# Optimization experiments

Hardware: AMD Instinct MI355X
Metric: run time of the kernel (lower is better)

## Reference

```python
import jax, jax.numpy as jnp
import numpy as np

MARGIN = 1.0
EPS = 1e-11


def setup_inputs() -> dict:
    key = jax.random.key(0)
    k1, k2, k3 = jax.random.split(key, 3)
    B, D, C = 8192, 512, 128
    features = jax.random.normal(k1, (B, D), dtype=jnp.float32)
    labels = jax.random.randint(k2, (B,), 0, C, dtype=jnp.int64)
    neg_u = jax.random.uniform(k3, (B,), dtype=jnp.float32)
    return {"features": features, "labels": labels, "neg_u": neg_u}


def reference(features, labels, neg_u):
    n = features.shape[0]
    sq = jnp.sum(features * features, axis=1)  # [n]
    d2 = sq[:, None] + sq[None, :] - 2.0 * (features @ features.T)
    dist = jnp.sqrt(jnp.clip(d2, EPS, None))  # [n, n]

    same = labels[:, None] == labels[None, :]
    eye = jnp.eye(n, dtype=bool)
    pos_mask = same & ~eye           # valid positives per anchor
    neg_mask = ~same                 # valid negatives per anchor
    n_neg = neg_mask.sum(axis=1)     # [n]

    # deterministic "random" negative: pick the floor(u * n_neg)-th negative
    # (stable argsort puts negatives first, preserving original order)
    order = jnp.argsort(jnp.where(neg_mask, 0, 1), axis=1, stable=True)  # [n, n]
    k = jnp.floor(neg_u * n_neg.astype(neg_u.dtype)).astype(jnp.int32)
    k = jnp.clip(k, 0, jnp.maximum(n_neg - 1, 0).astype(jnp.int32))
    neg_idx = jnp.take_along_axis(order, k[:, None], axis=1)[:, 0]       # [n]
    neg_dist = dist[jnp.arange(n), neg_idx]                               # [n]

    # MarginRankingLoss(y=1): max(0, margin + pos_dist - neg_dist), per (anchor, pos) pair
    valid = pos_mask & (n_neg > 0)[:, None]
    per_pair = jnp.maximum(MARGIN + dist - neg_dist[:, None], 0.0)
    counter = valid.sum()
    total = jnp.where(valid, per_pair, 0.0).sum()
    return total / counter.astype(total.dtype)
```

## Files before the change

### kernel.cpp

```cpp
#include <hip/hip_runtime.h>
#include <hip/hip_bf16.h>
#include <cstdint>

#define NN 8192
#define DD 512
#define NC 128

typedef unsigned short u16;
typedef __attribute__((ext_vector_type(8))) short short8;
typedef __attribute__((ext_vector_type(4))) float f32x4;

#define AS1 __attribute__((address_space(1)))
#define AS3 __attribute__((address_space(3)))

__device__ __forceinline__ float bf2f(short x) {
  return __uint_as_float(((unsigned)(unsigned short)x) << 16);
}

#define FB_OFF   ((size_t)0)
#define SQ_OFF   (FB_OFF + (size_t)NN*DD*2)
#define ND_OFF   (SQ_OFF + (size_t)NN*4)
#define ACC_OFF  (ND_OFF + (size_t)NN*4)
#define CC_OFF   (ACC_OFF + 64)
#define POS_OFF  (CC_OFF + 1024)

__global__ __launch_bounds__(256) void k_pc(const float* __restrict__ F,
    const int* __restrict__ labels, u16* __restrict__ Fb,
    float* __restrict__ sq, int* __restrict__ cc, int* __restrict__ pos) {
  const int wid = threadIdx.x >> 6, lane = threadIdx.x & 63;
  if (blockIdx.x < 2048) {
    const int row = blockIdx.x * 4 + wid;
    const float* fr = F + (size_t)row * DD + lane * 8;
    float4 v0 = *(const float4*)fr;
    float4 v1 = *(const float4*)(fr + 4);
    float s = v0.x*v0.x + v0.y*v0.y + v0.z*v0.z + v0.w*v0.w
            + v1.x*v1.x + v1.y*v1.y + v1.z*v1.z + v1.w*v1.w;
    #pragma unroll
    for (int o = 32; o; o >>= 1) s += __shfl_xor(s, o);
    float t[8] = {v0.x, v0.y, v0.z, v0.w, v1.x, v1.y, v1.z, v1.w};
    unsigned p[8];
    #pragma unroll
    for (int e = 0; e < 8; ++e) {
      unsigned b = __float_as_uint(t[e]);
      b += 0x7fffu + ((b >> 16) & 1u);
      p[e] = b >> 16;
    }
    uint4 w;
    w.x = p[0] | (p[1] << 16); w.y = p[2] | (p[3] << 16);
    w.z = p[4] | (p[5] << 16); w.w = p[6] | (p[7] << 16);
    *(uint4*)(Fb + (size_t)row * DD + lane * 8) = w;
    if (lane == 0) sq[row] = s;
  } else {
    const int c = blockIdx.x - 2048;
    __shared__ int wcnt[4], woff[4];
    const int base0 = wid * 2048;
    int cw = 0;
    for (int b = 0; b < 2048; b += 64)
      cw += __popcll(__ballot(labels[base0 + b + lane] == c));
    if (lane == 0) wcnt[wid] = cw;
    __syncthreads();
    if (threadIdx.x == 0) {
      int o = 0;
      #pragma unroll
      for (int w = 0; w < 4; ++w) { woff[w] = o; o += wcnt[w]; }
      cc[c] = o;
    }
    __syncthreads();
    int off = woff[wid];
    for (int b = 0; b < 2048; b += 64) {
      const int idx = base0 + b + lane;
      const int hit = (labels[idx] == c);
      const unsigned long long m = __ballot(hit);
      if (hit) pos[c * 128 + off + __popcll(m & ((1ull << lane) - 1ull))] = idx;
      off += __popcll(m);
    }
    __syncthreads();
    const int nc = cc[c];
    for (int t = nc + threadIdx.x; t < 128; t += 256) pos[c * 128 + t] = 0;
  }
}

__global__ __launch_bounds__(256) void k_neg2(const u16* __restrict__ Fb,
    const float* __restrict__ sq, const int* __restrict__ labels,
    const float* __restrict__ negu, const int* __restrict__ cc,
    const int* __restrict__ pos, float* __restrict__ nd,
    int* __restrict__ accz) {
  if (blockIdx.x == 0 && threadIdx.x < 16) accz[threadIdx.x] = 0;
  const int wid = threadIdx.x >> 6, lane = threadIdx.x & 63;
  const int i = blockIdx.x * 4 + wid;
  const int c = labels[i];
  const int nc = cc[c];
  const int n_neg = NN - nc;
  if (n_neg <= 0) { if (lane == 0) nd[i] = __builtin_inff(); return; }
  int k = (int)floorf(negu[i] * (float)n_neg);
  k = k < 0 ? 0 : (k > n_neg - 1 ? n_neg - 1 : k);
  const int* pc = pos + c * 128;
  const int p0 = pc[lane], p1 = pc[64 + lane];
  const int t = __popcll(__ballot((lane < nc) && (p0 - lane <= k)))
              + __popcll(__ballot((64 + lane < nc) && (p1 - (64 + lane) <= k)));
  const int j = k + t;
  const short8 av = *(const short8*)(Fb + (size_t)i * DD + lane * 8);
  const short8 bv = *(const short8*)(Fb + (size_t)j * DD + lane * 8);
  float d = 0.0f;
  #pragma unroll
  for (int e = 0; e < 8; ++e) d += bf2f(av[e]) * bf2f(bv[e]);
  #pragma unroll
  for (int o = 32; o; o >>= 1) d += __shfl_xor(d, o);
  if (lane == 0) nd[i] = sqrtf(fmaxf(sq[i] + sq[j] - 2.0f * d, 1e-11f));
}

__global__ __launch_bounds__(256) void k_cls(const u16* __restrict__ Fb,
    const float* __restrict__ sq, const float* __restrict__ nd,
    const int* __restrict__ cc, const int* __restrict__ pos,
    float* __restrict__ accf, float* __restrict__ out) {
  const int c = blockIdx.x >> 1, half = blockIdx.x & 1;
  __shared__ __align__(16) u16 P[128 * 512];
  __shared__ int posc[128];
  __shared__ float red[4];
  const int tid = threadIdx.x, wid = tid >> 6, lane = tid & 63;
  const int nc = cc[c];
  if (tid < 128) posc[tid] = pos[c * 128 + tid];
  __syncthreads();
  if (nc >= 2 && half * 64 < nc) {
    const int wr = half, wc = wid;
    const int r16 = lane & 15, gg = lane >> 4;
    const char* fb = (const char*)Fb;

    #pragma unroll 8
    for (int s = 0; s < 32; ++s) {
      const int row = wid * 32 + s;
      const int gr = posc[row];
      __builtin_amdgcn_global_load_lds(
          (const AS1 void*)(fb + (size_t)gr * 1024 + ((lane ^ (s & 7)) << 4)),
          (AS3 void*)(&P[row * 512]), 16, 0, 0);
    }

    f32x4 acc[4][2];
    #pragma unroll
    for (int m = 0; m < 4; ++m)
      #pragma unroll
      for (int n = 0; n < 2; ++n)
        #pragma unroll
        for (int q = 0; q < 4; ++q) acc[m][n][q] = 0.0f;

    __syncthreads();
    #pragma unroll 4
    for (int t = 0; t < 16; ++t) {
      short8 af[4], bf[2];
      #pragma unroll
      for (int m = 0; m < 4; ++m) {
        const int row = wr * 64 + m * 16 + r16;
        const int gl = (t * 4 + gg) ^ (row & 7);
        af[m] = *(const short8*)&P[row * 512 + gl * 8];
      }
      #pragma unroll
      for (int n = 0; n < 2; ++n) {
        const int row = wc * 32 + n * 16 + r16;
        const int gl = (t * 4 + gg) ^ (row & 7);
        bf[n] = *(const short8*)&P[row * 512 + gl * 8];
      }
      #pragma unroll
      for (int m = 0; m < 4; ++m)
        #pragma unroll
        for (int n = 0; n < 2; ++n)
          acc[m][n] = __builtin_amdgcn_mfma_f32_16x16x32_bf16(af[m], bf[n], acc[m][n], 0, 0, 0);
    }

    float lsum = 0.0f;
    int njv[2]; float sqj[2];
    #pragma unroll
    for (int n = 0; n < 2; ++n) {
      const int nj = wc * 32 + n * 16 + r16;
      njv[n] = nj; sqj[n] = sq[posc[nj]];
    }
    #pragma unroll
    for (int m = 0; m < 4; ++m) {
      #pragma unroll
      for (int q = 0; q < 4; ++q) {
        const int mi = wr * 64 + m * 16 + gg * 4 + q;
        const int i = posc[mi];
        const float sqi = sq[i], ndi = nd[i];
        const bool vi = mi < nc;
        #pragma unroll
        for (int n = 0; n < 2; ++n) {
          const float g = acc[m][n][q];
          const float dist = sqrtf(fmaxf(sqi + sqj[n] - 2.0f * g, 1e-11f));
          if (vi & (njv[n] < nc) & (mi != njv[n]))
            lsum += fmaxf(1.0f + dist - ndi, 0.0f);
        }
      }
    }
    #pragma unroll
    for (int o = 32; o; o >>= 1) lsum += __shfl_xor(lsum, o);
    if (lane == 0) red[wid] = lsum;
    __syncthreads();
    if (tid == 0) atomicAdd(accf, red[0] + red[1] + red[2] + red[3]);
  }
  if (tid == 0) {
    int* cnt  = (int*)accf + 1;
    int* done = (int*)accf + 2;
    if (half == 0 && nc < NN) atomicAdd(cnt, nc * (nc - 1));
    __threadfence();
    if (atomicAdd(done, 1) == 2 * NC - 1) {
      const float tot = atomicAdd(accf, 0.0f);
      const int n = atomicAdd(cnt, 0);
      out[0] = tot / (float)n;
    }
  }
}

extern "C" void kernel_launch(void* const* d_in, const int* in_sizes, int n_in,
                              void* d_out, int out_size, void* d_ws, size_t ws_size,
                              hipStream_t stream) {
  const float* F = (const float*)d_in[0];
  const int* labels = (const int*)d_in[1];
  const float* negu = (const float*)d_in[2];
  char* ws = (char*)d_ws;
  u16*   Fb    = (u16*)(ws + FB_OFF);
  float* sq    = (float*)(ws + SQ_OFF);
  float* nd    = (float*)(ws + ND_OFF);
  float* accf  = (float*)(ws + ACC_OFF);
  int*   cc    = (int*)(ws + CC_OFF);
  int*   pos   = (int*)(ws + POS_OFF);

  k_pc  <<<2048 + NC, 256, 0, stream>>>(F, labels, Fb, sq, cc, pos);
  k_neg2<<<NN / 4,    256, 0, stream>>>(Fb, sq, labels, negu, cc, pos, nd, (int*)accf);
  k_cls <<<2 * NC,    256, 0, stream>>>(Fb, sq, nd, cc, pos, accf, (float*)d_out);
}
```

Baseline: 35.68 us.

## Drop bf16 precompute pass; convert features on the fly in consumer kernels

```diff
diff --git a/kernel.cpp b/kernel.cpp
--- a/kernel.cpp
+++ b/kernel.cpp
@@ -13,79 +13,47 @@
 #define AS1 __attribute__((address_space(1)))
 #define AS3 __attribute__((address_space(3)))
 
-__device__ __forceinline__ float bf2f(short x) {
-  return __uint_as_float(((unsigned)(unsigned short)x) << 16);
-}
-
-#define FB_OFF   ((size_t)0)
-#define SQ_OFF   (FB_OFF + (size_t)NN*DD*2)
-#define ND_OFF   (SQ_OFF + (size_t)NN*4)
+#define ND_OFF   ((size_t)0)
 #define ACC_OFF  (ND_OFF + (size_t)NN*4)
 #define CC_OFF   (ACC_OFF + 64)
 #define POS_OFF  (CC_OFF + 1024)
 
-__global__ __launch_bounds__(256) void k_pc(const float* __restrict__ F,
-    const int* __restrict__ labels, u16* __restrict__ Fb,
-    float* __restrict__ sq, int* __restrict__ cc, int* __restrict__ pos) {
+__global__ __launch_bounds__(256) void k_pos(const int* __restrict__ labels,
+    int* __restrict__ cc, int* __restrict__ pos, int* __restrict__ accz) {
+  const int c = blockIdx.x;
   const int wid = threadIdx.x >> 6, lane = threadIdx.x & 63;
-  if (blockIdx.x < 2048) {
-    const int row = blockIdx.x * 4 + wid;
-    const float* fr = F + (size_t)row * DD + lane * 8;
-    float4 v0 = *(const float4*)fr;
-    float4 v1 = *(const float4*)(fr + 4);
-    float s = v0.x*v0.x + v0.y*v0.y + v0.z*v0.z + v0.w*v0.w
-            + v1.x*v1.x + v1.y*v1.y + v1.z*v1.z + v1.w*v1.w;
-    #pragma unroll
-    for (int o = 32; o; o >>= 1) s += __shfl_xor(s, o);
-    float t[8] = {v0.x, v0.y, v0.z, v0.w, v1.x, v1.y, v1.z, v1.w};
-    unsigned p[8];
-    #pragma unroll
-    for (int e = 0; e < 8; ++e) {
-      unsigned b = __float_as_uint(t[e]);
-      b += 0x7fffu + ((b >> 16) & 1u);
-      p[e] = b >> 16;
-    }
-    uint4 w;
-    w.x = p[0] | (p[1] << 16); w.y = p[2] | (p[3] << 16);
-    w.z = p[4] | (p[5] << 16); w.w = p[6] | (p[7] << 16);
-    *(uint4*)(Fb + (size_t)row * DD + lane * 8) = w;
-    if (lane == 0) sq[row] = s;
-  } else {
-    const int c = blockIdx.x - 2048;
-    __shared__ int wcnt[4], woff[4];
-    const int base0 = wid * 2048;
-    int cw = 0;
-    for (int b = 0; b < 2048; b += 64)
-      cw += __popcll(__ballot(labels[base0 + b + lane] == c));
-    if (lane == 0) wcnt[wid] = cw;
-    __syncthreads();
-    if (threadIdx.x == 0) {
-      int o = 0;
-      #pragma unroll
-      for (int w = 0; w < 4; ++w) { woff[w] = o; o += wcnt[w]; }
-      cc[c] = o;
-    }
-    __syncthreads();
-    int off = woff[wid];
-    for (int b = 0; b < 2048; b += 64) {
-      const int idx = base0 + b + lane;
-      const int hit = (labels[idx] == c);
-      const unsigned long long m = __ballot(hit);
-      if (hit) pos[c * 128 + off + __popcll(m & ((1ull << lane) - 1ull))] = idx;
-      off += __popcll(m);
-    }
-    __syncthreads();
-    const int nc = cc[c];
-    for (int t = nc + threadIdx.x; t < 128; t += 256) pos[c * 128 + t] = 0;
-  }
-}
-
-__global__ __launch_bounds__(256) void k_neg2(const u16* __restrict__ Fb,
-    const float* __restrict__ sq, const int* __restrict__ labels,
-    const float* __restrict__ negu, const int* __restrict__ cc,
-    const int* __restrict__ pos, float* __restrict__ nd,
-    int* __restrict__ accz) {
-  if (blockIdx.x == 0 && threadIdx.x < 16) accz[threadIdx.x] = 0;
+  if (c == 0 && threadIdx.x < 16) accz[threadIdx.x] = 0;
+  __shared__ int wcnt[4], woff[4];
+  const int base0 = wid * 2048;
+  int cw = 0;
+  for (int b = 0; b < 2048; b += 64)
+    cw += __popcll(__ballot(labels[base0 + b + lane] == c));
+  if (lane == 0) wcnt[wid] = cw;
+  __syncthreads();
+  if (threadIdx.x == 0) {
+    int o = 0;
+    #pragma unroll
+    for (int w = 0; w < 4; ++w) { woff[w] = o; o += wcnt[w]; }
+    cc[c] = o;
+  }
+  __syncthreads();
+  int off = woff[wid];
+  for (int b = 0; b < 2048; b += 64) {
+    const int idx = base0 + b + lane;
+    const int hit = (labels[idx] == c);
+    const unsigned long long m = __ballot(hit);
+    if (hit) pos[c * 128 + off + __popcll(m & ((1ull << lane) - 1ull))] = idx;
+    off += __popcll(m);
+  }
+  __syncthreads();
+  const int nc = cc[c];
+  for (int t = nc + threadIdx.x; t < 128; t += 256) pos[c * 128 + t] = 0;
+}
+
+__global__ __launch_bounds__(256) void k_neg(const float* __restrict__ F,
+    const int* __restrict__ labels, const float* __restrict__ negu,
+    const int* __restrict__ cc, const int* __restrict__ pos,
+    float* __restrict__ nd) {
   const int wid = threadIdx.x >> 6, lane = threadIdx.x & 63;
   const int i = blockIdx.x * 4 + wid;
   const int c = labels[i];
@@ -99,23 +67,31 @@
   const int t = __popcll(__ballot((lane < nc) && (p0 - lane <= k)))
               + __popcll(__ballot((64 + lane < nc) && (p1 - (64 + lane) <= k)));
   const int j = k + t;
-  const short8 av = *(const short8*)(Fb + (size_t)i * DD + lane * 8);
-  const short8 bv = *(const short8*)(Fb + (size_t)j * DD + lane * 8);
-  float d = 0.0f;
+  const float* fi = F + (size_t)i * DD + lane * 8;
+  const float* fj = F + (size_t)j * DD + lane * 8;
+  float4 a0 = *(const float4*)fi, a1 = *(const float4*)(fi + 4);
+  float4 b0 = *(const float4*)fj, b1 = *(const float4*)(fj + 4);
+  float d  = a0.x*b0.x + a0.y*b0.y + a0.z*b0.z + a0.w*b0.w
+           + a1.x*b1.x + a1.y*b1.y + a1.z*b1.z + a1.w*b1.w;
+  float si = a0.x*a0.x + a0.y*a0.y + a0.z*a0.z + a0.w*a0.w
+           + a1.x*a1.x + a1.y*a1.y + a1.z*a1.z + a1.w*a1.w;
+  float sj = b0.x*b0.x + b0.y*b0.y + b0.z*b0.z + b0.w*b0.w
+           + b1.x*b1.x + b1.y*b1.y + b1.z*b1.z + b1.w*b1.w;
   #pragma unroll
-  for (int e = 0; e < 8; ++e) d += bf2f(av[e]) * bf2f(bv[e]);
-  #pragma unroll
-  for (int o = 32; o; o >>= 1) d += __shfl_xor(d, o);
-  if (lane == 0) nd[i] = sqrtf(fmaxf(sq[i] + sq[j] - 2.0f * d, 1e-11f));
-}
-
-__global__ __launch_bounds__(256) void k_cls(const u16* __restrict__ Fb,
-    const float* __restrict__ sq, const float* __restrict__ nd,
-    const int* __restrict__ cc, const int* __restrict__ pos,
-    float* __restrict__ accf, float* __restrict__ out) {
+  for (int o = 32; o; o >>= 1) {
+    d += __shfl_xor(d, o); si += __shfl_xor(si, o); sj += __shfl_xor(sj, o);
+  }
+  if (lane == 0) nd[i] = sqrtf(fmaxf(si + sj - 2.0f * d, 1e-11f));
+}
+
+__global__ __launch_bounds__(256) void k_cls(const float* __restrict__ F,
+    const float* __restrict__ nd, const int* __restrict__ cc,
+    const int* __restrict__ pos, float* __restrict__ accf,
+    float* __restrict__ out) {
   const int c = blockIdx.x >> 1, half = blockIdx.x & 1;
   __shared__ __align__(16) u16 P[128 * 512];
   __shared__ int posc[128];
+  __shared__ float sqc[128], ndc[128];
   __shared__ float red[4];
   const int tid = threadIdx.x, wid = tid >> 6, lane = tid & 63;
   const int nc = cc[c];
@@ -124,15 +100,32 @@
   if (nc >= 2 && half * 64 < nc) {
     const int wr = half, wc = wid;
     const int r16 = lane & 15, gg = lane >> 4;
-    const char* fb = (const char*)Fb;
-
-    #pragma unroll 8
+
+    if (tid < 128) ndc[tid] = nd[posc[tid]];
+
+    #pragma unroll 4
     for (int s = 0; s < 32; ++s) {
       const int row = wid * 32 + s;
-      const int gr = posc[row];
-      __builtin_amdgcn_global_load_lds(
-          (const AS1 void*)(fb + (size_t)gr * 1024 + ((lane ^ (s & 7)) << 4)),
-          (AS3 void*)(&P[row * 512]), 16, 0, 0);
+      const float* fr = F + (size_t)posc[row] * DD + lane * 8;
+      float4 v0 = *(const float4*)fr;
+      float4 v1 = *(const float4*)(fr + 4);
+      float sp = v0.x*v0.x + v0.y*v0.y + v0.z*v0.z + v0.w*v0.w
+               + v1.x*v1.x + v1.y*v1.y + v1.z*v1.z + v1.w*v1.w;
+      #pragma unroll
+      for (int o = 32; o; o >>= 1) sp += __shfl_xor(sp, o);
+      if (lane == 0) sqc[row] = sp;
+      float t[8] = {v0.x, v0.y, v0.z, v0.w, v1.x, v1.y, v1.z, v1.w};
+      unsigned p[8];
+      #pragma unroll
+      for (int e = 0; e < 8; ++e) {
+        unsigned b = __float_as_uint(t[e]);
+        b += 0x7fffu + ((b >> 16) & 1u);
+        p[e] = b >> 16;
+      }
+      uint4 w;
+      w.x = p[0] | (p[1] << 16); w.y = p[2] | (p[3] << 16);
+      w.z = p[4] | (p[5] << 16); w.w = p[6] | (p[7] << 16);
+      *(uint4*)&P[row * 512 + ((lane ^ (row & 7)) << 3)] = w;
     }
 
     f32x4 acc[4][2];
@@ -171,15 +164,14 @@
     #pragma unroll
     for (int n = 0; n < 2; ++n) {
       const int nj = wc * 32 + n * 16 + r16;
-      njv[n] = nj; sqj[n] = sq[posc[nj]];
+      njv[n] = nj; sqj[n] = sqc[nj];
     }
     #pragma unroll
     for (int m = 0; m < 4; ++m) {
       #pragma unroll
       for (int q = 0; q < 4; ++q) {
         const int mi = wr * 64 + m * 16 + gg * 4 + q;
-        const int i = posc[mi];
-        const float sqi = sq[i], ndi = nd[i];
+        const float sqi = sqc[mi], ndi = ndc[mi];
         const bool vi = mi < nc;
         #pragma unroll
         for (int n = 0; n < 2; ++n) {
@@ -216,14 +208,12 @@
   const int* labels = (const int*)d_in[1];
   const float* negu = (const float*)d_in[2];
   char* ws = (char*)d_ws;
-  u16*   Fb    = (u16*)(ws + FB_OFF);
-  float* sq    = (float*)(ws + SQ_OFF);
   float* nd    = (float*)(ws + ND_OFF);
   float* accf  = (float*)(ws + ACC_OFF);
   int*   cc    = (int*)(ws + CC_OFF);
   int*   pos   = (int*)(ws + POS_OFF);
 
-  k_pc  <<<2048 + NC, 256, 0, stream>>>(F, labels, Fb, sq, cc, pos);
-  k_neg2<<<NN / 4,    256, 0, stream>>>(Fb, sq, labels, negu, cc, pos, nd, (int*)accf);
-  k_cls <<<2 * NC,    256, 0, stream>>>(Fb, sq, nd, cc, pos, accf, (float*)d_out);
-}
+  k_pos<<<NC,     256, 0, stream>>>(labels, cc, pos, (int*)accf);
+  k_neg<<<NN / 4, 256, 0, stream>>>(F, labels, negu, cc, pos, nd);
+  k_cls<<<2 * NC, 256, 0, stream>>>(F, nd, cc, pos, accf, (float*)d_out);
+}
```

Result: slower. 45.83 us (+28.4%).

## Split label bucketing into its own kernel and fuse negative-distance with bf16 conversion

Applied to the files above, without the earlier changes.

```diff
diff --git a/kernel.cpp b/kernel.cpp
--- a/kernel.cpp
+++ b/kernel.cpp
@@ -12,10 +12,6 @@
 
 #define AS1 __attribute__((address_space(1)))
 #define AS3 __attribute__((address_space(3)))
-
-__device__ __forceinline__ float bf2f(short x) {
-  return __uint_as_float(((unsigned)(unsigned short)x) << 16);
-}
 
 #define FB_OFF   ((size_t)0)
 #define SQ_OFF   (FB_OFF + (size_t)NN*DD*2)
@@ -24,9 +20,42 @@
 #define CC_OFF   (ACC_OFF + 64)
 #define POS_OFF  (CC_OFF + 1024)
 
-__global__ __launch_bounds__(256) void k_pc(const float* __restrict__ F,
-    const int* __restrict__ labels, u16* __restrict__ Fb,
-    float* __restrict__ sq, int* __restrict__ cc, int* __restrict__ pos) {
+__global__ __launch_bounds__(256) void k_pos(const int* __restrict__ labels,
+    int* __restrict__ cc, int* __restrict__ pos, int* __restrict__ accz) {
+  const int c = blockIdx.x;
+  const int wid = threadIdx.x >> 6, lane = threadIdx.x & 63;
+  if (c == 0 && threadIdx.x < 16) accz[threadIdx.x] = 0;
+  __shared__ int wcnt[4], woff[4];
+  const int base0 = wid * 2048;
+  int cw = 0;
+  for (int b = 0; b < 2048; b += 64)
+    cw += __popcll(__ballot(labels[base0 + b + lane] == c));
+  if (lane == 0) wcnt[wid] = cw;
+  __syncthreads();
+  if (threadIdx.x == 0) {
+    int o = 0;
+    #pragma unroll
+    for (int w = 0; w < 4; ++w) { woff[w] = o; o += wcnt[w]; }
+    cc[c] = o;
+  }
+  __syncthreads();
+  int off = woff[wid];
+  for (int b = 0; b < 2048; b += 64) {
+    const int idx = base0 + b + lane;
+    const int hit = (labels[idx] == c);
+    const unsigned long long m = __ballot(hit);
+    if (hit) pos[c * 128 + off + __popcll(m & ((1ull << lane) - 1ull))] = idx;
+    off += __popcll(m);
+  }
+  __syncthreads();
+  const int nc = cc[c];
+  for (int t = nc + threadIdx.x; t < 128; t += 256) pos[c * 128 + t] = 0;
+}
+
+__global__ __launch_bounds__(256) void k_pn(const float* __restrict__ F,
+    const int* __restrict__ labels, const float* __restrict__ negu,
+    const int* __restrict__ cc, const int* __restrict__ pos,
+    u16* __restrict__ Fb, float* __restrict__ sq, float* __restrict__ nd) {
   const int wid = threadIdx.x >> 6, lane = threadIdx.x & 63;
   if (blockIdx.x < 2048) {
     const int row = blockIdx.x * 4 + wid;
@@ -51,62 +80,34 @@
     *(uint4*)(Fb + (size_t)row * DD + lane * 8) = w;
     if (lane == 0) sq[row] = s;
   } else {
-    const int c = blockIdx.x - 2048;
-    __shared__ int wcnt[4], woff[4];
-    const int base0 = wid * 2048;
-    int cw = 0;
-    for (int b = 0; b < 2048; b += 64)
-      cw += __popcll(__ballot(labels[base0 + b + lane] == c));
-    if (lane == 0) wcnt[wid] = cw;
-    __syncthreads();
-    if (threadIdx.x == 0) {
-      int o = 0;
-      #pragma unroll
-      for (int w = 0; w < 4; ++w) { woff[w] = o; o += wcnt[w]; }
-      cc[c] = o;
-    }
-    __syncthreads();
-    int off = woff[wid];
-    for (int b = 0; b < 2048; b += 64) {
-      const int idx = base0 + b + lane;
-      const int hit = (labels[idx] == c);
-      const unsigned long long m = __ballot(hit);
-      if (hit) pos[c * 128 + off + __popcll(m & ((1ull << lane) - 1ull))] = idx;
-      off += __popcll(m);
-    }
-    __syncthreads();
+    const int i = (blockIdx.x - 2048) * 4 + wid;
+    const int c = labels[i];
     const int nc = cc[c];
-    for (int t = nc + threadIdx.x; t < 128; t += 256) pos[c * 128 + t] = 0;
-  }
-}
-
-__global__ __launch_bounds__(256) void k_neg2(const u16* __restrict__ Fb,
-    const float* __restrict__ sq, const int* __restrict__ labels,
-    const float* __restrict__ negu, const int* __restrict__ cc,
-    const int* __restrict__ pos, float* __restrict__ nd,
-    int* __restrict__ accz) {
-  if (blockIdx.x == 0 && threadIdx.x < 16) accz[threadIdx.x] = 0;
-  const int wid = threadIdx.x >> 6, lane = threadIdx.x & 63;
-  const int i = blockIdx.x * 4 + wid;
-  const int c = labels[i];
-  const int nc = cc[c];
-  const int n_neg = NN - nc;
-  if (n_neg <= 0) { if (lane == 0) nd[i] = __builtin_inff(); return; }
-  int k = (int)floorf(negu[i] * (float)n_neg);
-  k = k < 0 ? 0 : (k > n_neg - 1 ? n_neg - 1 : k);
-  const int* pc = pos + c * 128;
-  const int p0 = pc[lane], p1 = pc[64 + lane];
-  const int t = __popcll(__ballot((lane < nc) && (p0 - lane <= k)))
-              + __popcll(__ballot((64 + lane < nc) && (p1 - (64 + lane) <= k)));
-  const int j = k + t;
-  const short8 av = *(const short8*)(Fb + (size_t)i * DD + lane * 8);
-  const short8 bv = *(const short8*)(Fb + (size_t)j * DD + lane * 8);
-  float d = 0.0f;
-  #pragma unroll
-  for (int e = 0; e < 8; ++e) d += bf2f(av[e]) * bf2f(bv[e]);
-  #pragma unroll
-  for (int o = 32; o; o >>= 1) d += __shfl_xor(d, o);
-  if (lane == 0) nd[i] = sqrtf(fmaxf(sq[i] + sq[j] - 2.0f * d, 1e-11f));
+    const int n_neg = NN - nc;
+    if (n_neg <= 0) { if (lane == 0) nd[i] = __builtin_inff(); return; }
+    int k = (int)floorf(negu[i] * (float)n_neg);
+    k = k < 0 ? 0 : (k > n_neg - 1 ? n_neg - 1 : k);
+    const int* pc = pos + c * 128;
+    const int p0 = pc[lane], p1 = pc[64 + lane];
+    const int t = __popcll(__ballot((lane < nc) && (p0 - lane <= k)))
+                + __popcll(__ballot((64 + lane < nc) && (p1 - (64 + lane) <= k)));
+    const int j = k + t;
+    const float* fi = F + (size_t)i * DD + lane * 8;
+    const float* fj = F + (size_t)j * DD + lane * 8;
+    float4 a0 = *(const float4*)fi, a1 = *(const float4*)(fi + 4);
+    float4 b0 = *(const float4*)fj, b1 = *(const float4*)(fj + 4);
+    float d  = a0.x*b0.x + a0.y*b0.y + a0.z*b0.z + a0.w*b0.w
+             + a1.x*b1.x + a1.y*b1.y + a1.z*b1.z + a1.w*b1.w;
+    float si = a0.x*a0.x + a0.y*a0.y + a0.z*a0.z + a0.w*a0.w
+             + a1.x*a1.x + a1.y*a1.y + a1.z*a1.z + a1.w*a1.w;
+    float sj = b0.x*b0.x + b0.y*b0.y + b0.z*b0.z + b0.w*b0.w
+             + b1.x*b1.x + b1.y*b1.y + b1.z*b1.z + b1.w*b1.w;
+    #pragma unroll
+    for (int o = 32; o; o >>= 1) {
+      d += __shfl_xor(d, o); si += __shfl_xor(si, o); sj += __shfl_xor(sj, o);
+    }
+    if (lane == 0) nd[i] = sqrtf(fmaxf(si + sj - 2.0f * d, 1e-11f));
+  }
 }
 
 __global__ __launch_bounds__(256) void k_cls(const u16* __restrict__ Fb,
@@ -223,7 +224,7 @@
   int*   cc    = (int*)(ws + CC_OFF);
   int*   pos   = (int*)(ws + POS_OFF);
 
-  k_pc  <<<2048 + NC, 256, 0, stream>>>(F, labels, Fb, sq, cc, pos);
-  k_neg2<<<NN / 4,    256, 0, stream>>>(Fb, sq, labels, negu, cc, pos, nd, (int*)accf);
-  k_cls <<<2 * NC,    256, 0, stream>>>(Fb, sq, nd, cc, pos, accf, (float*)d_out);
-}
+  k_pos<<<NC,     256, 0, stream>>>(labels, cc, pos, (int*)accf);
+  k_pn <<<4096,   256, 0, stream>>>(F, labels, negu, cc, pos, Fb, sq, nd);
+  k_cls<<<2 * NC, 256, 0, stream>>>(Fb, sq, nd, cc, pos, accf, (float*)d_out);
+}
```

Result: faster. 34.31 us (-3.8%).

## Fuse negative-distance kernel into class kernel, overlapping it with LDS loads

Applied to the files above, without the earlier changes.

```diff
diff --git a/kernel.cpp b/kernel.cpp
--- a/kernel.cpp
+++ b/kernel.cpp
@@ -13,22 +13,19 @@
 #define AS1 __attribute__((address_space(1)))
 #define AS3 __attribute__((address_space(3)))
 
-__device__ __forceinline__ float bf2f(short x) {
-  return __uint_as_float(((unsigned)(unsigned short)x) << 16);
-}
-
 #define FB_OFF   ((size_t)0)
 #define SQ_OFF   (FB_OFF + (size_t)NN*DD*2)
-#define ND_OFF   (SQ_OFF + (size_t)NN*4)
-#define ACC_OFF  (ND_OFF + (size_t)NN*4)
+#define ACC_OFF  (SQ_OFF + (size_t)NN*4)
 #define CC_OFF   (ACC_OFF + 64)
 #define POS_OFF  (CC_OFF + 1024)
 
 __global__ __launch_bounds__(256) void k_pc(const float* __restrict__ F,
     const int* __restrict__ labels, u16* __restrict__ Fb,
-    float* __restrict__ sq, int* __restrict__ cc, int* __restrict__ pos) {
+    float* __restrict__ sq, int* __restrict__ cc, int* __restrict__ pos,
+    int* __restrict__ accz) {
   const int wid = threadIdx.x >> 6, lane = threadIdx.x & 63;
   if (blockIdx.x < 2048) {
+    if (blockIdx.x == 0 && threadIdx.x < 16) accz[threadIdx.x] = 0;
     const int row = blockIdx.x * 4 + wid;
     const float* fr = F + (size_t)row * DD + lane * 8;
     float4 v0 = *(const float4*)fr;
@@ -80,42 +77,15 @@
   }
 }
 
-__global__ __launch_bounds__(256) void k_neg2(const u16* __restrict__ Fb,
-    const float* __restrict__ sq, const int* __restrict__ labels,
+__global__ __launch_bounds__(256) void k_cls(const u16* __restrict__ Fb,
+    const float* __restrict__ F, const float* __restrict__ sq,
     const float* __restrict__ negu, const int* __restrict__ cc,
-    const int* __restrict__ pos, float* __restrict__ nd,
-    int* __restrict__ accz) {
-  if (blockIdx.x == 0 && threadIdx.x < 16) accz[threadIdx.x] = 0;
-  const int wid = threadIdx.x >> 6, lane = threadIdx.x & 63;
-  const int i = blockIdx.x * 4 + wid;
-  const int c = labels[i];
-  const int nc = cc[c];
-  const int n_neg = NN - nc;
-  if (n_neg <= 0) { if (lane == 0) nd[i] = __builtin_inff(); return; }
-  int k = (int)floorf(negu[i] * (float)n_neg);
-  k = k < 0 ? 0 : (k > n_neg - 1 ? n_neg - 1 : k);
-  const int* pc = pos + c * 128;
-  const int p0 = pc[lane], p1 = pc[64 + lane];
-  const int t = __popcll(__ballot((lane < nc) && (p0 - lane <= k)))
-              + __popcll(__ballot((64 + lane < nc) && (p1 - (64 + lane) <= k)));
-  const int j = k + t;
-  const short8 av = *(const short8*)(Fb + (size_t)i * DD + lane * 8);
-  const short8 bv = *(const short8*)(Fb + (size_t)j * DD + lane * 8);
-  float d = 0.0f;
-  #pragma unroll
-  for (int e = 0; e < 8; ++e) d += bf2f(av[e]) * bf2f(bv[e]);
-  #pragma unroll
-  for (int o = 32; o; o >>= 1) d += __shfl_xor(d, o);
-  if (lane == 0) nd[i] = sqrtf(fmaxf(sq[i] + sq[j] - 2.0f * d, 1e-11f));
-}
-
-__global__ __launch_bounds__(256) void k_cls(const u16* __restrict__ Fb,
-    const float* __restrict__ sq, const float* __restrict__ nd,
-    const int* __restrict__ cc, const int* __restrict__ pos,
-    float* __restrict__ accf, float* __restrict__ out) {
+    const int* __restrict__ pos, float* __restrict__ accf,
+    float* __restrict__ out) {
   const int c = blockIdx.x >> 1, half = blockIdx.x & 1;
   __shared__ __align__(16) u16 P[128 * 512];
-  __shared__ int posc[128];
+  __shared__ int posc[128], jm[64];
+  __shared__ float pd[64][4], ndc[64];
   __shared__ float red[4];
   const int tid = threadIdx.x, wid = tid >> 6, lane = tid & 63;
   const int nc = cc[c];
@@ -135,6 +105,34 @@
           (AS3 void*)(&P[row * 512]), 16, 0, 0);
     }
 
+    {
+      const int ml = tid >> 2, q = tid & 3;
+      const int row = half * 64 + ml;
+      if (row < nc) {
+        const int i = posc[row];
+        const int n_neg = NN - nc;
+        int k = (int)floorf(negu[i] * (float)n_neg);
+        k = k < 0 ? 0 : (k > n_neg - 1 ? n_neg - 1 : k);
+        int lo = 0, hi = nc;
+        while (lo < hi) {
+          const int mid = (lo + hi) >> 1;
+          if (posc[mid] - mid <= k) lo = mid + 1; else hi = mid;
+        }
+        const int j = k + lo;
+        if (q == 0) jm[ml] = j;
+        const float* fi = F + (size_t)i * DD + q * 128;
+        const float* fj = F + (size_t)j * DD + q * 128;
+        float d = 0.0f;
+        #pragma unroll 8
+        for (int e = 0; e < 32; ++e) {
+          const float4 a = ((const float4*)fi)[e];
+          const float4 b = ((const float4*)fj)[e];
+          d += a.x*b.x + a.y*b.y + a.z*b.z + a.w*b.w;
+        }
+        pd[ml][q] = d;
+      }
+    }
+
     f32x4 acc[4][2];
     #pragma unroll
     for (int m = 0; m < 4; ++m)
@@ -144,6 +142,14 @@
         for (int q = 0; q < 4; ++q) acc[m][n][q] = 0.0f;
 
     __syncthreads();
+    if (tid < 64) {
+      const int row = half * 64 + tid;
+      if (row < nc) {
+        const float d = pd[tid][0] + pd[tid][1] + pd[tid][2] + pd[tid][3];
+        ndc[tid] = sqrtf(fmaxf(sq[posc[row]] + sq[jm[tid]] - 2.0f * d, 1e-11f));
+      } else ndc[tid] = __builtin_inff();
+    }
+
     #pragma unroll 4
     for (int t = 0; t < 16; ++t) {
       short8 af[4], bf[2];
@@ -165,6 +171,7 @@
         for (int n = 0; n < 2; ++n)
           acc[m][n] = __builtin_amdgcn_mfma_f32_16x16x32_bf16(af[m], bf[n], acc[m][n], 0, 0, 0);
     }
+    __syncthreads();
 
     float lsum = 0.0f;
     int njv[2]; float sqj[2];
@@ -178,8 +185,8 @@
       #pragma unroll
       for (int q = 0; q < 4; ++q) {
         const int mi = wr * 64 + m * 16 + gg * 4 + q;
-        const int i = posc[mi];
-        const float sqi = sq[i], ndi = nd[i];
+        const float sqi = sq[posc[mi]];
+        const float ndi = ndc[mi - half * 64];
         const bool vi = mi < nc;
         #pragma unroll
         for (int n = 0; n < 2; ++n) {
@@ -218,12 +225,10 @@
   char* ws = (char*)d_ws;
   u16*   Fb    = (u16*)(ws + FB_OFF);
   float* sq    = (float*)(ws + SQ_OFF);
-  float* nd    = (float*)(ws + ND_OFF);
   float* accf  = (float*)(ws + ACC_OFF);
   int*   cc    = (int*)(ws + CC_OFF);
   int*   pos   = (int*)(ws + POS_OFF);
 
-  k_pc  <<<2048 + NC, 256, 0, stream>>>(F, labels, Fb, sq, cc, pos);
-  k_neg2<<<NN / 4,    256, 0, stream>>>(Fb, sq, labels, negu, cc, pos, nd, (int*)accf);
-  k_cls <<<2 * NC,    256, 0, stream>>>(Fb, sq, nd, cc, pos, accf, (float*)d_out);
+  k_pc <<<2048 + NC, 256, 0, stream>>>(F, labels, Fb, sq, cc, pos, (int*)accf);
+  k_cls<<<2 * NC,    256, 0, stream>>>(Fb, F, sq, negu, cc, pos, accf, (float*)d_out);
 }
```

New measurement: 35.46 us. About the same (-0.6%).
